# Optimization experiments

Measured on AMD Instinct MI355X. Metric: run time of the kernel, lower is better.

The kernel has to match this reference:

```python
import jax, jax.numpy as jnp
import numpy as np

T = 0.07          # temperature
K_POS = 5         # top-k positives per noun and for mask prediction
MARGIN = 0.1
LAM_CONTRAST = 0.6
LAM_MASK = 0.4


def _l2n(x):
    return x / jnp.linalg.norm(x, axis=-1, keepdims=True)


def setup_inputs() -> dict:
    key = jax.random.key(0)
    k0, k1, k2, k3 = jax.random.split(key, 4)
    B, N, D, M = 64, 576, 512, 16  # N = 24*24 patch grid
    patch_feats = _l2n(jax.random.normal(k0, (B, N, D), jnp.float32))
    noun_feats = _l2n(jax.random.normal(k1, (B, M, D), jnp.float32))
    global_img_feat = _l2n(jax.random.normal(k2, (B, D), jnp.float32))
    global_txt_feat = _l2n(jax.random.normal(k3, (B, D), jnp.float32))
    logit_scale = jnp.full((1,), 1.0 / 0.07, jnp.float32)
    idx = jnp.arange(B, dtype=jnp.int32)
    return {
        "patch_feats": patch_feats,
        "noun_feats": noun_feats,
        "global_img_feat": global_img_feat,
        "global_txt_feat": global_txt_feat,
        "logit_scale": logit_scale,
        "idx": idx,
    }


def _fine_grained_loss(patch_feats, noun_feats):
    # sim[b,m,n] = <noun_m, patch_n>; replaces the nested Python loops.
    B = patch_feats.shape[0]
    sim = jnp.einsum('bmd,bnd->bmn', noun_feats, patch_feats)
    scaled = sim / T
    # Per-noun contrastive loss. log_softmax over cat([topk, rest]) equals
    # log_softmax over all N entries evaluated at the topk positions, so:
    #   loss = -sum_topk log_softmax = K_POS*lse - sum(topk scaled values)
    lse = jax.nn.logsumexp(scaled, axis=-1)              # [B, M]
    topv, _ = jax.lax.top_k(scaled, K_POS)               # [B, M, K]
    contrast_loss = jnp.mean(K_POS * lse - topv.sum(-1))
    # Mask-prediction BCE loss (pool_type='mean').
    pooled = sim.mean(axis=1)                            # [B, N]
    _, tidx = jax.lax.top_k(pooled, K_POS)               # [B, K]
    pred = jnp.zeros_like(pooled).at[jnp.arange(B)[:, None], tidx].set(1.0)
    x = pooled / T
    mask_loss = jnp.mean(jnp.logaddexp(0.0, x) - x * pred)
    return LAM_CONTRAST * contrast_loss + LAM_MASK * mask_loss


def _contrastive_loss(img, txt, logit_scale, idx):
    logits = logit_scale.reshape(()) * (img @ txt.T)
    pos = (idx[:, None] == idx[None, :]).astype(logits.dtype)
    labels = pos / pos.sum(axis=1, keepdims=True)
    li2t = -(jax.nn.log_softmax(logits, axis=1) * labels).sum(1).mean()
    lt2i = -(jax.nn.log_softmax(logits.T, axis=1) * labels).sum(1).mean()
    return 0.5 * (li2t + lt2i)


def _triplet_loss(img, txt):
    scores = img @ txt.T
    d = jnp.diagonal(scores)
    eye = jnp.eye(scores.shape[0], dtype=bool)
    cost_s = jnp.where(eye, 0.0, jnp.clip(MARGIN + scores - d[:, None], 0.0)).sum()
    cost_im = jnp.where(eye, 0.0, jnp.clip(MARGIN + scores - d[None, :], 0.0)).sum()
    return 0.5 * (cost_s + cost_im)


def reference(patch_feats, noun_feats, global_img_feat, global_txt_feat, logit_scale, idx):
    loss_c = _contrastive_loss(global_img_feat, global_txt_feat, logit_scale, idx)
    loss_t = _triplet_loss(global_img_feat, global_txt_feat)
    loss_f = _fine_grained_loss(patch_feats, noun_feats)
    return jnp.stack([loss_c, loss_t, loss_f])
```

## Files before the change

kernel.cpp:

```cpp
#include <hip/hip_runtime.h>
#include <hip/hip_bf16.h>
#include <math.h>

#define NB 64
#define NN 576
#define ND 512
#define NM 16
#define QPB 9
#define NPB 64
#define NW 4
#define DPW 128
#define CH 32
#define NCHW 4
#define LSTR 36
#define WVF (NPB * LSTR)
#define KPOS 5
#define TINV 14.2857142857142857f

#define WS_REC_OFF 4096
#define RECSZ 144

#define FINF __builtin_inff()

__device__ __forceinline__ void ins5(float (&a)[5], float v) {
  if (v > a[4]) {
    a[4] = v;
    if (a[4] > a[3]) { float x = a[4]; a[4] = a[3]; a[3] = x; }
    if (a[3] > a[2]) { float x = a[3]; a[3] = a[2]; a[2] = x; }
    if (a[2] > a[1]) { float x = a[2]; a[2] = a[1]; a[1] = x; }
    if (a[1] > a[0]) { float x = a[1]; a[1] = a[0]; a[0] = x; }
  }
}

__device__ __forceinline__ void merge5(float (&a)[5], const float (&b)[5]) {
  float r[5];
#pragma unroll
  for (int k = 0; k < 5; ++k) {
    float best = -FINF;
#pragma unroll
    for (int i = 0; i <= k + 1; ++i) {
      const int j = k + 1 - i;
      const float av = (i == 0) ? FINF : a[i - 1];
      const float bv = (j == 0) ? FINF : b[j - 1];
      best = fmaxf(best, fminf(av, bv));
    }
    r[k] = best;
  }
#pragma unroll
  for (int k = 0; k < 5; ++k) a[k] = r[k];
}

__device__ __forceinline__ void merge5_shfl(float (&a)[5], int msk) {
  float o[5];
#pragma unroll
  for (int k = 0; k < 5; ++k) o[k] = __shfl_xor(a[k], msk, 64);
  merge5(a, o);
}

__global__ __launch_bounds__(256) void k_main(
    const float* __restrict__ patch, const float* __restrict__ noun,
    const float* __restrict__ gimg, const float* __restrict__ gtxt,
    float* __restrict__ ws) {
  const int blk = blockIdx.x;
  const int t = threadIdx.x;

  __shared__ float lds[NW * WVF + NM * 65];

  if (blk >= NB * QPB) {
    const int i = blk - NB * QPB;
    const int j = t & 63;
    const int qd = t >> 6;
    const float4* ip = (const float4*)(gimg + (size_t)i * ND + qd * DPW);
    const float4* tp = (const float4*)(gtxt + (size_t)j * ND + qd * DPW);
    float acc = 0.f;
#pragma unroll 8
    for (int q = 0; q < DPW / 4; ++q) {
      const float4 a = ip[q];
      const float4 b = tp[q];
      acc += a.x * b.x + a.y * b.y + a.z * b.z + a.w * b.w;
    }
    lds[qd * 64 + j] = acc;
    __syncthreads();
    if (t < 64) ws[i * 64 + t] = lds[t] + lds[64 + t] + lds[128 + t] + lds[192 + t];
    return;
  }

  const int b = blk / QPB;
  const int quad = blk - b * QPB;
  const int wv = __builtin_amdgcn_readfirstlane(t >> 6);
  const int lane = t & 63;

  const float* pbase = patch + ((size_t)b * NN + (size_t)quad * NPB) * ND + wv * DPW;
  const float* nbase = noun + (size_t)b * NM * ND + wv * DPW;
  float* wlds = &lds[wv * WVF];

  float acc[NM];
#pragma unroll
  for (int m = 0; m < NM; ++m) acc[m] = 0.f;

  const int sp = lane >> 3;
  const int sf = lane & 7;

  float4 stg[8];
#pragma unroll
  for (int r = 0; r < 8; ++r)
    stg[r] = *(const float4*)(pbase + (size_t)(8 * r + sp) * ND + sf * 4);

  for (int c = 0; c < NCHW; ++c) {
#pragma unroll
    for (int r = 0; r < 8; ++r)
      *(float4*)&wlds[(8 * r + sp) * LSTR + sf * 4] = stg[r];
    if (c + 1 < NCHW) {
      const float* pb2 = pbase + (size_t)(c + 1) * CH;
#pragma unroll
      for (int r = 0; r < 8; ++r)
        stg[r] = *(const float4*)(pb2 + (size_t)(8 * r + sp) * ND + sf * 4);
    }
    float pf[CH];
    {
      const float4* rowp = (const float4*)&wlds[lane * LSTR];
#pragma unroll
      for (int k = 0; k < 8; ++k) {
        const float4 v = rowp[k];
        pf[4 * k] = v.x; pf[4 * k + 1] = v.y; pf[4 * k + 2] = v.z; pf[4 * k + 3] = v.w;
      }
    }
    const float* nc = nbase + c * CH;
#pragma unroll 4
    for (int m = 0; m < NM; ++m) {
      const float* np_ = nc + m * ND;
      float s0 = 0.f, s1 = 0.f;
#pragma unroll
      for (int d = 0; d < CH; d += 2) {
        s0 += pf[d] * np_[d];
        s1 += pf[d + 1] * np_[d + 1];
      }
      acc[m] += s0 + s1;
    }
  }

  __syncthreads();
#pragma unroll
  for (int m = 0; m < NM; ++m) lds[wv * 1024 + m * 64 + lane] = acc[m];
  __syncthreads();
  {
    const int m = t >> 4;
    const int p0 = (t & 15) * 4;
    float* simL = &lds[NW * WVF];
#pragma unroll
    for (int i2 = 0; i2 < 4; ++i2) {
      const int p = p0 + i2;
      const float s = (lds[m * 64 + p] + lds[1024 + m * 64 + p] +
                       lds[2048 + m * 64 + p] + lds[3072 + m * 64 + p]) * TINV;
      simL[m * 65 + p] = s;
    }
  }
  __syncthreads();

  float* simL = &lds[NW * WVF];
  float* rec = ws + WS_REC_OFF + (size_t)blk * RECSZ;

  if (wv == 1) {
    float x = 0.f;
#pragma unroll
    for (int m = 0; m < NM; ++m) x += simL[m * 65 + lane];
    x *= (1.f / 16.f);
    float sxp = (x > 0.f) ? (x + log1pf(expf(-x))) : log1pf(expf(x));
    float t5[5] = {x, -FINF, -FINF, -FINF, -FINF};
#pragma unroll
    for (int msk = 1; msk < 64; msk <<= 1) {
      sxp += __shfl_xor(sxp, msk, 64);
      merge5_shfl(t5, msk);
    }
    if (lane == 0) {
      rec[128] = sxp;
#pragma unroll
      for (int k = 0; k < 5; ++k) rec[129 + k] = t5[k];
    }
  } else if (wv == 0) {
    const int rr_ = lane & 15;
    const int h = lane >> 4;
    const float* row = &simL[rr_ * 65 + h * 16];
    float mx = -FINF;
#pragma unroll
    for (int k = 0; k < 16; ++k) mx = fmaxf(mx, row[k]);
    mx = fmaxf(mx, __shfl_xor(mx, 16, 64));
    mx = fmaxf(mx, __shfl_xor(mx, 32, 64));
    float se = 0.f;
    float r5[5] = {-FINF, -FINF, -FINF, -FINF, -FINF};
#pragma unroll
    for (int k = 0; k < 16; ++k) {
      const float v = row[k];
      se += expf(v - mx);
      ins5(r5, v);
    }
    se += __shfl_xor(se, 16, 64);
    se += __shfl_xor(se, 32, 64);
    merge5_shfl(r5, 16);
    merge5_shfl(r5, 32);
    if (h == 0) {
      float* rr = rec + rr_ * 8;
      rr[0] = mx;
      rr[1] = se;
#pragma unroll
      for (int k = 0; k < 5; ++k) rr[2 + k] = r5[k];
    }
  }
}

__global__ __launch_bounds__(64) void k_final(
    const float* __restrict__ ws, const float* __restrict__ lscale,
    const int* __restrict__ idx, float* __restrict__ out) {
  const int blk = blockIdx.x;
  const int t = threadIdx.x;

  if (blk < NB) {
    const float* base = ws + WS_REC_OFF + (size_t)blk * QPB * RECSZ;
    const int m = t & 15;
    const int g = t >> 4;
    const int nq = (g == 0) ? 3 : 2;

    float lm[3], ls[3];
    float t5[5] = {-FINF, -FINF, -FINF, -FINF, -FINF};
#pragma unroll
    for (int i = 0; i < 3; ++i) { lm[i] = -FINF; ls[i] = 0.f; }
    float mx = -FINF;
    for (int i = 0; i < nq; ++i) {
      const float* rr = base + (g + 4 * i) * RECSZ + m * 8;
      lm[i] = rr[0]; ls[i] = rr[1];
      mx = fmaxf(mx, rr[0]);
#pragma unroll
      for (int k = 0; k < 5; ++k) ins5(t5, rr[2 + k]);
    }
    mx = fmaxf(mx, __shfl_xor(mx, 16, 64));
    mx = fmaxf(mx, __shfl_xor(mx, 32, 64));
    float S = 0.f;
    for (int i = 0; i < nq; ++i) S += ls[i] * expf(lm[i] - mx);
    S += __shfl_xor(S, 16, 64);
    S += __shfl_xor(S, 32, 64);
    merge5_shfl(t5, 16);
    merge5_shfl(t5, 32);

    float contrib = 0.f;
    if (g == 0) {
      const float lse = mx + logf(S);
      const float st = t5[0] + t5[1] + t5[2] + t5[3] + t5[4];
      contrib = (KPOS * lse - st) * (0.6f / (float)(NB * NM));
    }

    float sp_ = 0.f;
    float u5[5] = {-FINF, -FINF, -FINF, -FINF, -FINF};
    if (m == 0) {
      for (int i = 0; i < nq; ++i) {
        const float* rr = base + (g + 4 * i) * RECSZ + 128;
        sp_ += rr[0];
#pragma unroll
        for (int k = 0; k < 5; ++k) ins5(u5, rr[1 + k]);
      }
    }
    sp_ += __shfl_xor(sp_, 16, 64);
    sp_ += __shfl_xor(sp_, 32, 64);
    merge5_shfl(u5, 16);
    merge5_shfl(u5, 32);
    if (t == 0) {
      const float st = u5[0] + u5[1] + u5[2] + u5[3] + u5[4];
      contrib += (sp_ - st) * (0.4f / (float)(NB * NN));
    }
#pragma unroll
    for (int msk = 1; msk < 64; msk <<= 1) contrib += __shfl_xor(contrib, msk, 64);
    if (t == 0) atomicAdd(out + 2, contrib);
    return;
  }

  __shared__ float s[64 * 65];
  __shared__ float dg[64];
  __shared__ int idl[64];
  for (int i = 0; i < 64; ++i) s[i * 65 + t] = ws[i * 64 + t];
  idl[t] = idx[t];
  __syncthreads();
  dg[t] = s[t * 66];
  __syncthreads();
  const float sc = lscale[0];

  float mR = -FINF, mC = -FINF;
  for (int j = 0; j < 64; ++j) {
    mR = fmaxf(mR, sc * s[t * 65 + j]);
    mC = fmaxf(mC, sc * s[j * 65 + t]);
  }
  float seR = 0.f, seC = 0.f;
  for (int j = 0; j < 64; ++j) {
    seR += expf(sc * s[t * 65 + j] - mR);
    seC += expf(sc * s[j * 65 + t] - mC);
  }
  const float lseR = mR + logf(seR);
  const float lseC = mC + logf(seC);

  const int myid = idl[t];
  const float di = dg[t];
  float ps = 0.f, trow = 0.f, tcol = 0.f, cs = 0.f, ci = 0.f;
  for (int j = 0; j < 64; ++j) {
    const float sv = s[t * 65 + j];
    const float svT = s[j * 65 + t];
    if (idl[j] == myid) {
      ps += 1.f;
      trow += sc * sv - lseR;
      tcol += sc * svT - lseC;
    }
    if (j != t) {
      cs += fmaxf(0.f, 0.1f + sv - di);
      ci += fmaxf(0.f, 0.1f + sv - dg[j]);
    }
  }
  float vc = -(trow + tcol) / ps;
  float vt = cs + ci;
#pragma unroll
  for (int msk = 1; msk < 64; msk <<= 1) {
    vc += __shfl_xor(vc, msk, 64);
    vt += __shfl_xor(vt, msk, 64);
  }
  if (t == 0) {
    out[0] = vc * (0.5f / 64.f);
    out[1] = vt * 0.5f;
  }
}

extern "C" void kernel_launch(void* const* d_in, const int* in_sizes, int n_in,
                              void* d_out, int out_size, void* d_ws, size_t ws_size,
                              hipStream_t stream) {
  const float* patch = (const float*)d_in[0];
  const float* noun  = (const float*)d_in[1];
  const float* gimg  = (const float*)d_in[2];
  const float* gtxt  = (const float*)d_in[3];
  const float* lsc   = (const float*)d_in[4];
  const int*   idx   = (const int*)d_in[5];
  float* out = (float*)d_out;
  float* ws  = (float*)d_ws;

  hipMemsetAsync(d_out, 0, 3 * sizeof(float), stream);
  k_main<<<dim3(NB * QPB + NB), dim3(256), 0, stream>>>(patch, noun, gimg, gtxt, ws);
  k_final<<<dim3(NB + 1), dim3(64), 0, stream>>>(ws, lsc, idx, out);
}
```

Measured before the change: 150.2 us.

## Compute noun-patch similarity with bf16 MFMA and a noun pre-conversion kernel

```diff
diff --git a/kernel.cpp b/kernel.cpp
--- a/kernel.cpp
+++ b/kernel.cpp
@@ -7,20 +7,32 @@
 #define ND 512
 #define NM 16
 #define QPB 9
-#define NPB 64
-#define NW 4
-#define DPW 128
-#define CH 32
-#define NCHW 4
-#define LSTR 36
-#define WVF (NPB * LSTR)
 #define KPOS 5
 #define TINV 14.2857142857142857f
 
+#define NFINE (NB * QPB)
+#define NBLK1 (NFINE + NB)
 #define WS_REC_OFF 4096
 #define RECSZ 144
+#define WS_NOUNF (WS_REC_OFF + NFINE * RECSZ)
 
 #define FINF __builtin_inff()
+
+typedef __attribute__((ext_vector_type(8))) short short8;
+typedef __attribute__((ext_vector_type(4))) float floatx4;
+
+__device__ __forceinline__ unsigned pk2(float lo, float hi) {
+  return __builtin_amdgcn_perm(__float_as_uint(hi), __float_as_uint(lo), 0x07060302u);
+}
+
+__device__ __forceinline__ short8 packB(const float4 a, const float4 b) {
+  union { unsigned u[4]; short8 s; } cv;
+  cv.u[0] = pk2(a.x, a.y);
+  cv.u[1] = pk2(a.z, a.w);
+  cv.u[2] = pk2(b.x, b.y);
+  cv.u[3] = pk2(b.z, b.w);
+  return cv.s;
+}
 
 __device__ __forceinline__ void ins5(float (&a)[5], float v) {
   if (v > a[4]) {
@@ -57,154 +69,121 @@
   merge5(a, o);
 }
 
-__global__ __launch_bounds__(256) void k_main(
-    const float* __restrict__ patch, const float* __restrict__ noun,
-    const float* __restrict__ gimg, const float* __restrict__ gtxt,
-    float* __restrict__ ws) {
+__global__ __launch_bounds__(256) void k_prep(
+    const float* __restrict__ noun, float* __restrict__ ws) {
+  const int i = blockIdx.x * 256 + threadIdx.x;
+  const float4 v = ((const float4*)noun)[i];
+  unsigned ux = __float_as_uint(v.x), uy = __float_as_uint(v.y);
+  unsigned uz = __float_as_uint(v.z), uw = __float_as_uint(v.w);
+  ux += 0x7FFFu + ((ux >> 16) & 1u);
+  uy += 0x7FFFu + ((uy >> 16) & 1u);
+  uz += 0x7FFFu + ((uz >> 16) & 1u);
+  uw += 0x7FFFu + ((uw >> 16) & 1u);
+  uint2 o;
+  o.x = __builtin_amdgcn_perm(uy, ux, 0x07060302u);
+  o.y = __builtin_amdgcn_perm(uw, uz, 0x07060302u);
+  ((uint2*)((unsigned short*)(ws + WS_NOUNF)))[i] = o;
+}
+
+__global__ __launch_bounds__(256) void k_sim(
+    const float* __restrict__ patch, const float* __restrict__ gimg,
+    const float* __restrict__ gtxt, float* __restrict__ ws) {
   const int blk = blockIdx.x;
   const int t = threadIdx.x;
-
-  __shared__ float lds[NW * WVF + NM * 65];
-
-  if (blk >= NB * QPB) {
-    const int i = blk - NB * QPB;
-    const int j = t & 63;
-    const int qd = t >> 6;
-    const float4* ip = (const float4*)(gimg + (size_t)i * ND + qd * DPW);
-    const float4* tp = (const float4*)(gtxt + (size_t)j * ND + qd * DPW);
-    float acc = 0.f;
-#pragma unroll 8
-    for (int q = 0; q < DPW / 4; ++q) {
-      const float4 a = ip[q];
-      const float4 b = tp[q];
-      acc += a.x * b.x + a.y * b.y + a.z * b.z + a.w * b.w;
-    }
-    lds[qd * 64 + j] = acc;
+  const int lane = t & 63;
+
+  __shared__ float S[NM * 65];
+
+  if (blk < NFINE) {
+    const int b = blk / QPB, quad = blk - b * QPB;
+    const int w = t >> 6;
+    const int nidx = lane & 15;
+    const int k0 = (lane >> 4) * 8;
+
+    const unsigned short* nrow =
+        (const unsigned short*)(ws + WS_NOUNF) + ((size_t)b * NM + nidx) * ND + k0;
+    const float* prow =
+        patch + ((size_t)(b * NN + quad * 64 + w * 16 + nidx)) * ND + k0;
+
+    floatx4 acc = {0.f, 0.f, 0.f, 0.f};
+#pragma unroll 4
+    for (int ks = 0; ks < 16; ++ks) {
+      const int o = ks * 32;
+      const short8 af = *(const short8*)(nrow + o);
+      const float4 p0 = *(const float4*)(prow + o);
+      const float4 p1 = *(const float4*)(prow + o + 4);
+      const short8 bf = packB(p0, p1);
+      acc = __builtin_amdgcn_mfma_f32_16x16x32_bf16(af, bf, acc, 0, 0, 0);
+    }
+
+    const int mrow = (lane >> 4) * 4;
+    const int pcol = w * 16 + nidx;
+#pragma unroll
+    for (int r = 0; r < 4; ++r) S[(mrow + r) * 65 + pcol] = acc[r] * TINV;
     __syncthreads();
-    if (t < 64) ws[i * 64 + t] = lds[t] + lds[64 + t] + lds[128 + t] + lds[192 + t];
-    return;
-  }
-
-  const int b = blk / QPB;
-  const int quad = blk - b * QPB;
-  const int wv = __builtin_amdgcn_readfirstlane(t >> 6);
-  const int lane = t & 63;
-
-  const float* pbase = patch + ((size_t)b * NN + (size_t)quad * NPB) * ND + wv * DPW;
-  const float* nbase = noun + (size_t)b * NM * ND + wv * DPW;
-  float* wlds = &lds[wv * WVF];
-
-  float acc[NM];
-#pragma unroll
-  for (int m = 0; m < NM; ++m) acc[m] = 0.f;
-
-  const int sp = lane >> 3;
-  const int sf = lane & 7;
-
-  float4 stg[8];
-#pragma unroll
-  for (int r = 0; r < 8; ++r)
-    stg[r] = *(const float4*)(pbase + (size_t)(8 * r + sp) * ND + sf * 4);
-
-  for (int c = 0; c < NCHW; ++c) {
-#pragma unroll
-    for (int r = 0; r < 8; ++r)
-      *(float4*)&wlds[(8 * r + sp) * LSTR + sf * 4] = stg[r];
-    if (c + 1 < NCHW) {
-      const float* pb2 = pbase + (size_t)(c + 1) * CH;
-#pragma unroll
-      for (int r = 0; r < 8; ++r)
-        stg[r] = *(const float4*)(pb2 + (size_t)(8 * r + sp) * ND + sf * 4);
-    }
-    float pf[CH];
-    {
-      const float4* rowp = (const float4*)&wlds[lane * LSTR];
-#pragma unroll
-      for (int k = 0; k < 8; ++k) {
-        const float4 v = rowp[k];
-        pf[4 * k] = v.x; pf[4 * k + 1] = v.y; pf[4 * k + 2] = v.z; pf[4 * k + 3] = v.w;
-      }
-    }
-    const float* nc = nbase + c * CH;
-#pragma unroll 4
-    for (int m = 0; m < NM; ++m) {
-      const float* np_ = nc + m * ND;
-      float s0 = 0.f, s1 = 0.f;
-#pragma unroll
-      for (int d = 0; d < CH; d += 2) {
-        s0 += pf[d] * np_[d];
-        s1 += pf[d + 1] * np_[d + 1];
-      }
-      acc[m] += s0 + s1;
-    }
-  }
-
-  __syncthreads();
-#pragma unroll
-  for (int m = 0; m < NM; ++m) lds[wv * 1024 + m * 64 + lane] = acc[m];
-  __syncthreads();
-  {
-    const int m = t >> 4;
-    const int p0 = (t & 15) * 4;
-    float* simL = &lds[NW * WVF];
-#pragma unroll
-    for (int i2 = 0; i2 < 4; ++i2) {
-      const int p = p0 + i2;
-      const float s = (lds[m * 64 + p] + lds[1024 + m * 64 + p] +
-                       lds[2048 + m * 64 + p] + lds[3072 + m * 64 + p]) * TINV;
-      simL[m * 65 + p] = s;
-    }
-  }
-  __syncthreads();
-
-  float* simL = &lds[NW * WVF];
-  float* rec = ws + WS_REC_OFF + (size_t)blk * RECSZ;
-
-  if (wv == 1) {
-    float x = 0.f;
-#pragma unroll
-    for (int m = 0; m < NM; ++m) x += simL[m * 65 + lane];
-    x *= (1.f / 16.f);
-    float sxp = (x > 0.f) ? (x + log1pf(expf(-x))) : log1pf(expf(x));
-    float t5[5] = {x, -FINF, -FINF, -FINF, -FINF};
-#pragma unroll
-    for (int msk = 1; msk < 64; msk <<= 1) {
-      sxp += __shfl_xor(sxp, msk, 64);
-      merge5_shfl(t5, msk);
-    }
-    if (lane == 0) {
-      rec[128] = sxp;
-#pragma unroll
-      for (int k = 0; k < 5; ++k) rec[129 + k] = t5[k];
-    }
-  } else if (wv == 0) {
-    const int rr_ = lane & 15;
-    const int h = lane >> 4;
-    const float* row = &simL[rr_ * 65 + h * 16];
-    float mx = -FINF;
-#pragma unroll
-    for (int k = 0; k < 16; ++k) mx = fmaxf(mx, row[k]);
-    mx = fmaxf(mx, __shfl_xor(mx, 16, 64));
-    mx = fmaxf(mx, __shfl_xor(mx, 32, 64));
-    float se = 0.f;
-    float r5[5] = {-FINF, -FINF, -FINF, -FINF, -FINF};
-#pragma unroll
-    for (int k = 0; k < 16; ++k) {
-      const float v = row[k];
-      se += expf(v - mx);
-      ins5(r5, v);
-    }
-    se += __shfl_xor(se, 16, 64);
-    se += __shfl_xor(se, 32, 64);
-    merge5_shfl(r5, 16);
-    merge5_shfl(r5, 32);
-    if (h == 0) {
-      float* rr = rec + rr_ * 8;
-      rr[0] = mx;
-      rr[1] = se;
-#pragma unroll
-      for (int k = 0; k < 5; ++k) rr[2 + k] = r5[k];
-    }
+
+    float* rec = ws + WS_REC_OFF + (size_t)blk * RECSZ;
+    if (w == 1) {
+      float x = 0.f;
+#pragma unroll
+      for (int m = 0; m < NM; ++m) x += S[m * 65 + lane];
+      x *= (1.f / 16.f);
+      float sxp = (x > 0.f) ? (x + log1pf(expf(-x))) : log1pf(expf(x));
+      float t5[5] = {x, -FINF, -FINF, -FINF, -FINF};
+#pragma unroll
+      for (int msk = 1; msk < 64; msk <<= 1) {
+        sxp += __shfl_xor(sxp, msk, 64);
+        merge5_shfl(t5, msk);
+      }
+      if (lane == 0) {
+        rec[128] = sxp;
+#pragma unroll
+        for (int k = 0; k < 5; ++k) rec[129 + k] = t5[k];
+      }
+    } else if (w == 0) {
+      const int r_ = lane & 15;
+      const int h = lane >> 4;
+      const float* row = &S[r_ * 65 + h * 16];
+      float mx = -FINF;
+#pragma unroll
+      for (int k = 0; k < 16; ++k) mx = fmaxf(mx, row[k]);
+      mx = fmaxf(mx, __shfl_xor(mx, 16, 64));
+      mx = fmaxf(mx, __shfl_xor(mx, 32, 64));
+      float se = 0.f;
+      float r5[5] = {-FINF, -FINF, -FINF, -FINF, -FINF};
+#pragma unroll
+      for (int k = 0; k < 16; ++k) {
+        const float v = row[k];
+        se += expf(v - mx);
+        ins5(r5, v);
+      }
+      se += __shfl_xor(se, 16, 64);
+      se += __shfl_xor(se, 32, 64);
+      merge5_shfl(r5, 16);
+      merge5_shfl(r5, 32);
+      if (h == 0) {
+        float* rr = rec + r_ * 8;
+        rr[0] = mx;
+        rr[1] = se;
+#pragma unroll
+        for (int k = 0; k < 5; ++k) rr[2 + k] = r5[k];
+      }
+    }
+  } else {
+    const int i = blk - NFINE;
+    const int dq = t >> 6;
+    const float4* ip = (const float4*)(gimg + (size_t)i * ND + dq * 128);
+    const float4* tp = (const float4*)(gtxt + (size_t)lane * ND + dq * 128);
+    float a = 0.f;
+#pragma unroll
+    for (int q = 0; q < 32; ++q) {
+      const float4 x = ip[q];
+      const float4 y = tp[q];
+      a += x.x * y.x + x.y * y.y + x.z * y.z + x.w * y.w;
+    }
+    S[dq * 64 + lane] = a;
+    __syncthreads();
+    if (t < 64) ws[i * 64 + t] = S[t] + S[64 + t] + S[128 + t] + S[192 + t];
   }
 }
 
@@ -337,6 +316,7 @@
   float* ws  = (float*)d_ws;
 
   hipMemsetAsync(d_out, 0, 3 * sizeof(float), stream);
-  k_main<<<dim3(NB * QPB + NB), dim3(256), 0, stream>>>(patch, noun, gimg, gtxt, ws);
+  k_prep<<<dim3(512), dim3(256), 0, stream>>>(noun, ws);
+  k_sim<<<dim3(NBLK1), dim3(256), 0, stream>>>(patch, gimg, gtxt, ws);
   k_final<<<dim3(NB + 1), dim3(64), 0, stream>>>(ws, lsc, idx, out);
 }
```

Measured after the change: 136.1 us. -9.4%, faster.
